# Optimization experiments

Measured on AMD Instinct MI355X. Metric: run time of the kernel, lower is better.

Reference implementation:

```python
import jax, jax.numpy as jnp
import numpy as np
import math

N_HEAD = 16
N_EMBD = 1024
HEAD_D = N_EMBD // N_HEAD
BASE = 10000


def rope(Y):
    # Y: [b, h, t, d]; positions start at 1 as in the torch code
    d = Y.shape[-1]
    t = Y.shape[-2]
    theta = BASE ** (-2.0 * jnp.arange(d // 2, dtype=Y.dtype) / d)
    theta2 = jnp.concatenate([theta, theta], axis=0)          # [d]
    pos = jnp.arange(1, t + 1, dtype=Y.dtype)                 # [t]
    C = pos[:, None] * theta2[None, :]                        # [t, d]
    cos, sin = jnp.cos(C), jnp.sin(C)
    Y2 = jnp.concatenate([-Y[..., d // 2:], Y[..., : d // 2]], axis=-1)
    return Y * cos + Y2 * sin


def setup_inputs() -> dict:
    key = jax.random.key(0)
    ks = jax.random.split(key, 9)
    s = 0.02
    x = jax.random.normal(ks[0], (4, 2048, N_EMBD), dtype=jnp.float32)
    Wq = jax.random.normal(ks[1], (N_EMBD, N_EMBD), dtype=jnp.float32) * s
    bq = jnp.zeros((N_EMBD,), dtype=jnp.float32)
    Wk = jax.random.normal(ks[2], (N_EMBD, N_EMBD), dtype=jnp.float32) * s
    bk = jnp.zeros((N_EMBD,), dtype=jnp.float32)
    Wv = jax.random.normal(ks[3], (N_EMBD, N_EMBD), dtype=jnp.float32) * s
    bv = jnp.zeros((N_EMBD,), dtype=jnp.float32)
    Wo = jax.random.normal(ks[4], (N_EMBD, N_EMBD), dtype=jnp.float32) * s
    bo = jnp.zeros((N_EMBD,), dtype=jnp.float32)
    return {"x": x, "Wq": Wq, "bq": bq, "Wk": Wk, "bk": bk,
            "Wv": Wv, "bv": bv, "Wo": Wo, "bo": bo}


def reference(x, Wq, bq, Wk, bk, Wv, bv, Wo, bo):
    b, t, _ = x.shape
    def split_heads(y):
        return y.reshape(b, t, N_HEAD, HEAD_D).transpose(0, 2, 1, 3)  # b h t d
    q = split_heads(x @ Wq.T + bq)
    k = split_heads(x @ Wk.T + bk)
    v = split_heads(x @ Wv.T + bv)
    q, k = rope(q), rope(k)
    scale = math.sqrt(HEAD_D)
    att = jnp.einsum('bhqd,bhkd->bhqk', q, k) / scale
    mask = jnp.tril(jnp.ones((t, t), dtype=bool))
    att = jnp.where(mask, att, -jnp.inf)
    att = jax.nn.softmax(att, axis=-1)
    y = jnp.einsum('bhqk,bhkd->bhqd', att, v)
    y = y.transpose(0, 2, 1, 3).reshape(b, t, N_EMBD)
    return y @ Wo.T + bo
```

## Files before the change

kernel.cpp:

```cpp
#include <hip/hip_runtime.h>
#include <hip/hip_bf16.h>
#include <cstdint>

typedef __attribute__((ext_vector_type(8))) short short8;
typedef __attribute__((ext_vector_type(4))) short short4v;
typedef __attribute__((ext_vector_type(4))) float f32x4;
typedef __attribute__((ext_vector_type(16))) float f32x16;
typedef __attribute__((ext_vector_type(4))) unsigned int u32x4;
typedef unsigned short ushort_t;
typedef unsigned int uint32;

#define DEVI static __device__ __forceinline__

DEVI ushort_t f2bf(float f){
  uint32 u = __builtin_bit_cast(uint32, f);
  u += 0x7FFFu + ((u >> 16) & 1u);
  return (ushort_t)(u >> 16);
}
DEVI float bf2f(ushort_t s){
  uint32 u = ((uint32)s) << 16;
  return __builtin_bit_cast(float, u);
}
DEVI uint32 cvtpk_bf16(float lo, float hi){
  uint32 r;
  asm("v_cvt_pk_bf16_f32 %0, %1, %2" : "=v"(r) : "v"(lo), "v"(hi));
  return r;
}
DEVI void plswap(uint32& a, uint32& b){
  asm("v_permlane32_swap_b32 %0, %1" : "+v"(a), "+v"(b));
}

typedef __attribute__((address_space(1))) const uint32 g_u32;
typedef __attribute__((address_space(3))) uint32 l_u32;
#define GL_LDS16(gp, lp) __builtin_amdgcn_global_load_lds((g_u32*)(gp), (l_u32*)(lp), 16, 0, 0)

__global__ __launch_bounds__(256) void convert_all(
    const float* __restrict__ x, const float* __restrict__ wq, const float* __restrict__ wk,
    const float* __restrict__ wv, const float* __restrict__ wo,
    ushort_t* __restrict__ xb, ushort_t* __restrict__ wqkv, ushort_t* __restrict__ wob){
  int bid = blockIdx.x;
  const float* src; ushort_t* dst; long base;
  if (bid < 4096){ src = x; dst = xb; base = (long)bid * 2048; }
  else {
    int r = bid - 4096; int sel = r >> 9; int o = r & 511;
    src = sel==0?wq: sel==1?wk: sel==2?wv: wo;
    dst = (sel<3) ? (wqkv + (long)sel * 1048576) : wob;
    base = (long)o * 2048;
  }
  long i = base + (long)threadIdx.x * 8;
  const float* p = src + i;
  float4 a = *(const float4*)p;
  float4 b = *(const float4*)(p + 4);
  short8 v;
  v[0]=(short)f2bf(a.x); v[1]=(short)f2bf(a.y); v[2]=(short)f2bf(a.z); v[3]=(short)f2bf(a.w);
  v[4]=(short)f2bf(b.x); v[5]=(short)f2bf(b.y); v[6]=(short)f2bf(b.z); v[7]=(short)f2bf(b.w);
  *(short8*)(dst + i) = v;
}

__global__ __launch_bounds__(256) void rope_table(float2* __restrict__ tab){
  const int idx = blockIdx.x * 256 + threadIdx.x;
  const int tok = idx >> 5, j = idx & 31;
  const float theta = exp2f(-(float)j * 0.4152410118609203f);
  const float ang = (float)(tok + 1) * theta;
  float s, c;
  sincosf(ang, &s, &c);
  tab[idx] = make_float2(c, s);
}

__global__ __launch_bounds__(256) void gemm_qkv(
    const ushort_t* __restrict__ A, const ushort_t* __restrict__ Bw,
    const float* __restrict__ bq, const float* __restrict__ bk, const float* __restrict__ bv,
    const float2* __restrict__ tab,
    ushort_t* __restrict__ Qb, ushort_t* __restrict__ Kb, ushort_t* __restrict__ Vt){
  __shared__ ushort_t As[4096];
  __shared__ ushort_t Bs[4096];
  const int tid = threadIdx.x, l = tid & 63, w = tid >> 6;
  const int lr = l & 15, lg = l >> 4;
  const int bid = (blockIdx.x & 7) * 192 + (blockIdx.x >> 3);
  const int bm = bid / 24, bn = bid % 24;
  const int m0 = bm << 7, n0 = bn << 7;
  const int wm = (w >> 1) << 6, wn = (w & 1) << 6;
  f32x4 acc[4][4] = {};
  const ushort_t* aS = A + (long)(m0 + (tid >> 2)) * 1024 + (tid & 3) * 8;
  const ushort_t* bS = Bw + (long)(n0 + (tid >> 2)) * 1024 + (tid & 3) * 8;
  const long skip = (long)64 * 1024;
  for (int kt = 0; kt < 32; ++kt){
    GL_LDS16(aS,        &As[w * 512]);
    GL_LDS16(aS + skip, &As[2048 + w * 512]);
    GL_LDS16(bS,        &Bs[w * 512]);
    GL_LDS16(bS + skip, &Bs[2048 + w * 512]);
    aS += 32; bS += 32;
    __syncthreads();
    short8 af[4], bfr[4];
#pragma unroll
    for (int mi = 0; mi < 4; ++mi) af[mi]  = *(const short8*)&As[(wm + mi*16 + lr)*32 + lg*8];
#pragma unroll
    for (int ni = 0; ni < 4; ++ni) bfr[ni] = *(const short8*)&Bs[(wn + ni*16 + lr)*32 + lg*8];
#pragma unroll
    for (int mi = 0; mi < 4; ++mi)
#pragma unroll
      for (int ni = 0; ni < 4; ++ni)
        acc[mi][ni] = __builtin_amdgcn_mfma_f32_16x16x32_bf16(af[mi], bfr[ni], acc[mi][ni], 0, 0, 0);
    __syncthreads();
  }
  const int sel = bn >> 3;
  const int h = ((n0 + wn) >> 6) & 15;
  const int colBase = n0 + wn + lr;
  if (sel < 2){
    ushort_t* dst = (sel == 0) ? Qb : Kb;
    const float* bp = (sel == 0) ? bq : bk;
    const float bvs[4] = {bp[colBase], bp[colBase+16], bp[colBase+32], bp[colBase+48]};
#pragma unroll
    for (int mi = 0; mi < 4; ++mi){
      const int row0 = m0 + wm + mi*16 + lg*4;
#pragma unroll
      for (int i = 0; i < 4; ++i){
        const int r = row0 + i;
        const int b = r >> 11, tok = r & 2047;
#pragma unroll
        for (int nip = 0; nip < 2; ++nip){
          const int j = lr + nip*16;
          const float2 cs = tab[tok*32 + j];
          const float v0 = acc[mi][nip][i]   + bvs[nip];
          const float v1 = acc[mi][nip+2][i] + bvs[nip+2];
          const long base = (((long)(b*16 + h) * 2048 + tok) << 6) + j;
          dst[base]      = f2bf(v0 * cs.x - v1 * cs.y);
          dst[base + 32] = f2bf(v1 * cs.x + v0 * cs.y);
        }
      }
    }
  } else {
    const float bvs[4] = {bv[colBase], bv[colBase+16], bv[colBase+32], bv[colBase+48]};
#pragma unroll
    for (int mi = 0; mi < 4; ++mi){
      const int row0 = m0 + wm + mi*16 + lg*4;
#pragma unroll
      for (int ni = 0; ni < 4; ++ni){
        const int d = lr + ni*16;
#pragma unroll
        for (int i = 0; i < 4; ++i){
          const int r = row0 + i;
          const int b = r >> 11, tok = r & 2047;
          Vt[((long)(b*16 + h) * 64 + d) * 2048 + tok] = f2bf(acc[mi][ni][i] + bvs[ni]);
        }
      }
    }
  }
}

__global__ __launch_bounds__(256) void gemm_out(
    const ushort_t* __restrict__ A, const ushort_t* __restrict__ Bw,
    const float* __restrict__ bias, float* __restrict__ Cout){
  __shared__ ushort_t As[4096];
  __shared__ ushort_t Bs[4096];
  const int tid = threadIdx.x, l = tid & 63, w = tid >> 6;
  const int lr = l & 15, lg = l >> 4;
  const int bid = (blockIdx.x & 7) * 64 + (blockIdx.x >> 3);
  const int bm = bid >> 3, bn = bid & 7;
  const int m0 = bm << 7, n0 = bn << 7;
  const int wm = (w >> 1) << 6, wn = (w & 1) << 6;
  f32x4 acc[4][4] = {};
  const ushort_t* aS = A + (long)(m0 + (tid >> 2)) * 1024 + (tid & 3) * 8;
  const ushort_t* bS = Bw + (long)(n0 + (tid >> 2)) * 1024 + (tid & 3) * 8;
  const long skip = (long)64 * 1024;
  for (int kt = 0; kt < 32; ++kt){
    GL_LDS16(aS,        &As[w * 512]);
    GL_LDS16(aS + skip, &As[2048 + w * 512]);
    GL_LDS16(bS,        &Bs[w * 512]);
    GL_LDS16(bS + skip, &Bs[2048 + w * 512]);
    aS += 32; bS += 32;
    __syncthreads();
    short8 af[4], bfr[4];
#pragma unroll
    for (int mi = 0; mi < 4; ++mi) af[mi]  = *(const short8*)&As[(wm + mi*16 + lr)*32 + lg*8];
#pragma unroll
    for (int ni = 0; ni < 4; ++ni) bfr[ni] = *(const short8*)&Bs[(wn + ni*16 + lr)*32 + lg*8];
#pragma unroll
    for (int mi = 0; mi < 4; ++mi)
#pragma unroll
      for (int ni = 0; ni < 4; ++ni)
        acc[mi][ni] = __builtin_amdgcn_mfma_f32_16x16x32_bf16(af[mi], bfr[ni], acc[mi][ni], 0, 0, 0);
    __syncthreads();
  }
  const int colBase = n0 + wn + lr;
#pragma unroll
  for (int mi = 0; mi < 4; ++mi){
    const int row0 = m0 + wm + mi*16 + lg*4;
#pragma unroll
    for (int ni = 0; ni < 4; ++ni){
      const int col = colBase + ni*16;
      const float bvv = bias[col];
#pragma unroll
      for (int i = 0; i < 4; ++i)
        Cout[(long)(row0 + i) * 1024 + col] = acc[mi][ni][i] + bvv;
    }
  }
}

__global__ __launch_bounds__(512, 4) void attn(
    const ushort_t* __restrict__ Qb, const ushort_t* __restrict__ Kb,
    const ushort_t* __restrict__ Vt, ushort_t* __restrict__ yb){
  __shared__ __align__(16) ushort_t Ks[2][2048];
  __shared__ __align__(16) ushort_t Vs[2][2048];
  const int tid = threadIdx.x;
  const int w = tid >> 6, l = tid & 63;
  const int lq = l & 31;
  const int hi = l >> 5;
  const int xcd = blockIdx.x & 7;
  const int idx = blockIdx.x >> 3;
  const int hi5 = idx >> 5;
  const int bh  = (xcd << 3) + ((idx >> 3) & 3) + hi5 * 4;
  const int qj  = hi5 ? (idx & 7) : 7 - (idx & 7);
  const int qc = (qj << 3) + w;
  const int q0 = qc << 5;
  const int ktmax = (qj << 3) + 7;
  const ushort_t* Qh = Qb + (long)bh * 2048 * 64;
  const ushort_t* Kh = Kb + (long)bh * 2048 * 64;
  const ushort_t* Vth = Vt + (long)bh * 64 * 2048;
  const int h8 = hi * 8;

  const ushort_t* qp = &Qh[(long)(q0 + lq) * 64 + h8];
  short8 qf0 = *(const short8*)(qp);
  short8 qf1 = *(const short8*)(qp + 16);
  short8 qf2 = *(const short8*)(qp + 32);
  short8 qf3 = *(const short8*)(qp + 48);

  const int stg_is_v = (w >= 4);
  long stg_src_off; int stg_dst_off;
  if (!stg_is_v){
    const int row = (w << 3) + (l >> 3);
    const int cl  = (l & 7) ^ (row & 7);
    stg_src_off = ((long)row << 6) + (cl << 3);
    stg_dst_off = (w << 9) + (l << 3);
  } else {
    const int row = ((w - 4) << 3) + (l >> 3);
    const int cl  = (l & 7) ^ (row & 7);
    const int dd  = row + ((cl & 4) << 3);
    stg_src_off = ((long)dd << 11) + ((cl & 3) << 3);
    stg_dst_off = ((w - 4) << 9) + (l << 3);
  }

  f32x16 o0 = {}, o1 = {};
  float lsum = 0.f;
  const float cl2 = 0.1803368801111204f;

  if (!stg_is_v) GL_LDS16(Kh + stg_src_off,  &Ks[0][stg_dst_off]);
  else           GL_LDS16(Vth + stg_src_off, &Vs[0][stg_dst_off]);
  __syncthreads();

  int cur = 0;
  for (int kt = 0; kt <= ktmax; ++kt){
    if (kt < ktmax){
      const int k0n = (kt + 1) << 5;
      if (!stg_is_v) GL_LDS16(Kh + ((long)k0n << 6) + stg_src_off, &Ks[cur ^ 1][stg_dst_off]);
      else           GL_LDS16(Vth + k0n + stg_src_off,             &Vs[cur ^ 1][stg_dst_off]);
    }
    if (kt <= qc){
      const int swk = lq & 7;
      const ushort_t* kr = &Ks[cur][lq << 6];
      short8 kf0 = *(const short8*)&kr[((hi    ) ^ swk) << 3];
      short8 kf1 = *(const short8*)&kr[((2 + hi) ^ swk) << 3];
      short8 kf2 = *(const short8*)&kr[((4 + hi) ^ swk) << 3];
      short8 kf3 = *(const short8*)&kr[((6 + hi) ^ swk) << 3];
      const ushort_t* vr = &Vs[cur][lq << 6];
      short8 vf00 = *(const short8*)&vr[((hi    ) ^ swk) << 3];
      short8 vf01 = *(const short8*)&vr[((2 + hi) ^ swk) << 3];
      short8 vf10 = *(const short8*)&vr[((4 + hi) ^ swk) << 3];
      short8 vf11 = *(const short8*)&vr[((6 + hi) ^ swk) << 3];
      f32x16 s = {};
      s = __builtin_amdgcn_mfma_f32_32x32x16_bf16(kf0, qf0, s, 0, 0, 0);
      s = __builtin_amdgcn_mfma_f32_32x32x16_bf16(kf1, qf1, s, 0, 0, 0);
      s = __builtin_amdgcn_mfma_f32_32x32x16_bf16(kf2, qf2, s, 0, 0, 0);
      s = __builtin_amdgcn_mfma_f32_32x32x16_bf16(kf3, qf3, s, 0, 0, 0);
      if (kt == qc){
#pragma unroll
        for (int r = 0; r < 16; ++r){
          const int rk = (r & 3) + 8 * (r >> 2) + 4 * hi;
          if (rk > lq) s[r] = -1e30f;
        }
      }
#pragma unroll
      for (int r = 0; r < 16; ++r) s[r] = __builtin_amdgcn_exp2f(__builtin_fmaf(s[r], cl2, -2.0f));
      {
        float t0 = (s[0] + s[1]) + (s[2] + s[3]);
        float t1 = (s[4] + s[5]) + (s[6] + s[7]);
        float t2 = (s[8] + s[9]) + (s[10] + s[11]);
        float t3 = (s[12] + s[13]) + (s[14] + s[15]);
        lsum += (t0 + t1) + (t2 + t3);
      }
      uint32 a0 = cvtpk_bf16(s[0], s[1]),  b0 = cvtpk_bf16(s[4], s[5]);
      uint32 a1 = cvtpk_bf16(s[2], s[3]),  b1 = cvtpk_bf16(s[6], s[7]);
      uint32 a2 = cvtpk_bf16(s[8], s[9]),  b2 = cvtpk_bf16(s[12], s[13]);
      uint32 a3 = cvtpk_bf16(s[10], s[11]),b3 = cvtpk_bf16(s[14], s[15]);
      plswap(a0, b0);
      plswap(a1, b1);
      plswap(a2, b2);
      plswap(a3, b3);
      u32x4 pc0 = {a0, a1, b0, b1};
      u32x4 pc1 = {a2, a3, b2, b3};
      short8 pb0 = __builtin_bit_cast(short8, pc0);
      short8 pb1 = __builtin_bit_cast(short8, pc1);
      o0 = __builtin_amdgcn_mfma_f32_32x32x16_bf16(vf00, pb0, o0, 0, 0, 0);
      o0 = __builtin_amdgcn_mfma_f32_32x32x16_bf16(vf01, pb1, o0, 0, 0, 0);
      o1 = __builtin_amdgcn_mfma_f32_32x32x16_bf16(vf10, pb0, o1, 0, 0, 0);
      o1 = __builtin_amdgcn_mfma_f32_32x32x16_bf16(vf11, pb1, o1, 0, 0, 0);
    }
    __syncthreads();
    cur ^= 1;
  }
  lsum += __shfl_xor(lsum, 32);
  const float inv = 1.0f / lsum;
  const int b = bh >> 4, h = bh & 15;
  const int tok = q0 + lq;
  ushort_t* yrow = yb + (long)(b * 2048 + tok) * 1024 + h * 64;
#pragma unroll
  for (int g = 0; g < 4; ++g){
    short4v p0, p1;
#pragma unroll
    for (int j = 0; j < 4; ++j){
      p0[j] = (short)f2bf(o0[4*g + j] * inv);
      p1[j] = (short)f2bf(o1[4*g + j] * inv);
    }
    *(short4v*)&yrow[8*g + 4*hi]      = p0;
    *(short4v*)&yrow[32 + 8*g + 4*hi] = p1;
  }
}

extern "C" void kernel_launch(void* const* d_in, const int* in_sizes, int n_in,
                              void* d_out, int out_size, void* d_ws, size_t ws_size,
                              hipStream_t stream){
  const float* x  = (const float*)d_in[0];
  const float* Wq = (const float*)d_in[1];
  const float* bq = (const float*)d_in[2];
  const float* Wk = (const float*)d_in[3];
  const float* bk = (const float*)d_in[4];
  const float* Wv = (const float*)d_in[5];
  const float* bv = (const float*)d_in[6];
  const float* Wo = (const float*)d_in[7];
  const float* bo = (const float*)d_in[8];
  char* ws = (char*)d_ws;
  ushort_t* xb   = (ushort_t*)(ws);
  ushort_t* wqkv = (ushort_t*)(ws + 16777216);
  ushort_t* wob  = (ushort_t*)(ws + 23068672);
  float2*   tab  = (float2*)  (ws + 25165824);
  ushort_t* Qb   = (ushort_t*)(ws + 25690112);
  ushort_t* Kb   = (ushort_t*)(ws + 42467328);
  ushort_t* Vt   = (ushort_t*)(ws + 59244544);
  ushort_t* yb   = xb;

  convert_all<<<6144, 256, 0, stream>>>(x, Wq, Wk, Wv, Wo, xb, wqkv, wob);
  rope_table<<<256, 256, 0, stream>>>(tab);
  gemm_qkv<<<1536, 256, 0, stream>>>(xb, wqkv, bq, bk, bv, tab, Qb, Kb, Vt);
  attn<<<512, 512, 0, stream>>>(Qb, Kb, Vt, yb);
  gemm_out<<<512, 256, 0, stream>>>(yb, wob, bo, (float*)d_out);
}
```

Measured before the change: 170.8 us.

## Rewrite QKV GEMM with 256x256 tiles, triple-buffered LDS and swizzle

Replaces the 128x128 QKV projection GEMM with a 256x256-tile kernel of 512 threads (8 waves) that triple-buffers its LDS stages. It issues global-to-LDS loads two k-steps ahead, splits each k-step into two MFMA phases with barriers and s_setprio, and XOR-swizzles the LDS layout to avoid bank conflicts. The aim is better reuse of each loaded tile and overlap of memory latency with compute. It uses about 96KB of LDS and more accumulator registers per thread, which limits occupancy, and gives fewer blocks (384) across the CUs.

```diff
diff --git a/kernel.cpp b/kernel.cpp
--- a/kernel.cpp
+++ b/kernel.cpp
@@ -67,81 +67,114 @@
   tab[idx] = make_float2(c, s);
 }
 
-__global__ __launch_bounds__(256) void gemm_qkv(
+__global__ __launch_bounds__(512, 2) void gemm256_qkv(
     const ushort_t* __restrict__ A, const ushort_t* __restrict__ Bw,
     const float* __restrict__ bq, const float* __restrict__ bk, const float* __restrict__ bv,
     const float2* __restrict__ tab,
     ushort_t* __restrict__ Qb, ushort_t* __restrict__ Kb, ushort_t* __restrict__ Vt){
-  __shared__ ushort_t As[4096];
-  __shared__ ushort_t Bs[4096];
-  const int tid = threadIdx.x, l = tid & 63, w = tid >> 6;
-  const int lr = l & 15, lg = l >> 4;
-  const int bid = (blockIdx.x & 7) * 192 + (blockIdx.x >> 3);
-  const int bm = bid / 24, bn = bid % 24;
-  const int m0 = bm << 7, n0 = bn << 7;
-  const int wm = (w >> 1) << 6, wn = (w & 1) << 6;
-  f32x4 acc[4][4] = {};
-  const ushort_t* aS = A + (long)(m0 + (tid >> 2)) * 1024 + (tid & 3) * 8;
-  const ushort_t* bS = Bw + (long)(n0 + (tid >> 2)) * 1024 + (tid & 3) * 8;
-  const long skip = (long)64 * 1024;
-  for (int kt = 0; kt < 32; ++kt){
-    GL_LDS16(aS,        &As[w * 512]);
-    GL_LDS16(aS + skip, &As[2048 + w * 512]);
-    GL_LDS16(bS,        &Bs[w * 512]);
-    GL_LDS16(bS + skip, &Bs[2048 + w * 512]);
-    aS += 32; bS += 32;
-    __syncthreads();
-    short8 af[4], bfr[4];
-#pragma unroll
-    for (int mi = 0; mi < 4; ++mi) af[mi]  = *(const short8*)&As[(wm + mi*16 + lr)*32 + lg*8];
-#pragma unroll
-    for (int ni = 0; ni < 4; ++ni) bfr[ni] = *(const short8*)&Bs[(wn + ni*16 + lr)*32 + lg*8];
-#pragma unroll
-    for (int mi = 0; mi < 4; ++mi)
-#pragma unroll
-      for (int ni = 0; ni < 4; ++ni)
-        acc[mi][ni] = __builtin_amdgcn_mfma_f32_16x16x32_bf16(af[mi], bfr[ni], acc[mi][ni], 0, 0, 0);
-    __syncthreads();
-  }
-  const int sel = bn >> 3;
-  const int h = ((n0 + wn) >> 6) & 15;
-  const int colBase = n0 + wn + lr;
+  __shared__ __align__(16) ushort_t S[49152];
+  const int tid = threadIdx.x;
+  const int w = tid >> 6, l = tid & 63, lr = l & 15, lg = l >> 4;
+  const int wm = w >> 2, wn = w & 3;
+  const int bid = (blockIdx.x & 7) * 48 + (blockIdx.x >> 3);
+  const int bm = bid / 12, bn = bid % 12;
+  const int m0 = bm << 8, n0 = bn << 8;
+  const int srow = tid >> 2;
+  const int swzc = (tid & 3) ^ (srow & 3) ^ ((srow >> 2) & 3);
+  const ushort_t* aS = A  + (long)(m0 + srow) * 1024 + swzc * 8;
+  const ushort_t* bS = Bw + (long)(n0 + srow) * 1024 + swzc * 8;
+  const int sw = (lr & 3) ^ ((lr >> 2) & 3);
+  const int aOff = ((wm << 7) + lr) * 32 + ((lg ^ sw) << 3);
+  const int bOff = 8192 + ((wn << 6) + lr) * 32 + ((lg ^ sw) << 3);
+  f32x4 acc[8][4] = {};
+
+#define STG(matOff, src, t, bf_) do{ \
+    GL_LDS16((src) + (long)(t)*32,          &S[(bf_)*16384 + (matOff) + tid*8]); \
+    GL_LDS16((src) + (long)(t)*32 + 131072, &S[(bf_)*16384 + (matOff) + 4096 + tid*8]); }while(0)
+
+  STG(0, aS, 0, 0); STG(8192, bS, 0, 0);
+  STG(0, aS, 1, 1); STG(8192, bS, 1, 1);
+  asm volatile("s_waitcnt vmcnt(4)" ::: "memory");
+  __builtin_amdgcn_s_barrier();
+
+  int buf = 0;
+  for (int t = 0; t < 32; ++t){
+    const int nbuf = (buf == 0) ? 2 : buf - 1;
+    const ushort_t* Sb = &S[buf * 16384];
+    short8 af[8], bf0[2];
+#pragma unroll
+    for (int mi = 0; mi < 8; ++mi) af[mi] = *(const short8*)&Sb[aOff + mi * 512];
+    bf0[0] = *(const short8*)&Sb[bOff];
+    bf0[1] = *(const short8*)&Sb[bOff + 512];
+    if (t < 30) STG(0, aS, t + 2, nbuf);
+    __builtin_amdgcn_s_barrier();
+    __builtin_amdgcn_s_setprio(1);
+#pragma unroll
+    for (int mi = 0; mi < 8; ++mi){
+      acc[mi][0] = __builtin_amdgcn_mfma_f32_16x16x32_bf16(af[mi], bf0[0], acc[mi][0], 0, 0, 0);
+      acc[mi][1] = __builtin_amdgcn_mfma_f32_16x16x32_bf16(af[mi], bf0[1], acc[mi][1], 0, 0, 0);
+    }
+    __builtin_amdgcn_s_setprio(0);
+    __builtin_amdgcn_s_barrier();
+    short8 bf1[2];
+    bf1[0] = *(const short8*)&Sb[bOff + 1024];
+    bf1[1] = *(const short8*)&Sb[bOff + 1536];
+    if (t < 30) STG(8192, bS, t + 2, nbuf);
+    __builtin_amdgcn_s_barrier();
+    __builtin_amdgcn_s_setprio(1);
+#pragma unroll
+    for (int mi = 0; mi < 8; ++mi){
+      acc[mi][2] = __builtin_amdgcn_mfma_f32_16x16x32_bf16(af[mi], bf1[0], acc[mi][2], 0, 0, 0);
+      acc[mi][3] = __builtin_amdgcn_mfma_f32_16x16x32_bf16(af[mi], bf1[1], acc[mi][3], 0, 0, 0);
+    }
+    __builtin_amdgcn_s_setprio(0);
+    if (t < 30) asm volatile("s_waitcnt vmcnt(4)" ::: "memory");
+    else        asm volatile("s_waitcnt vmcnt(0)" ::: "memory");
+    __builtin_amdgcn_s_barrier();
+    buf = (buf == 2) ? 0 : buf + 1;
+  }
+#undef STG
+
+  const int colX = n0 + (wn << 6);
+  const int sel = colX >> 10;
+  const int h = (colX >> 6) & 15;
+  const int cB = (colX & 1023) + lr;
   if (sel < 2){
-    ushort_t* dst = (sel == 0) ? Qb : Kb;
-    const float* bp = (sel == 0) ? bq : bk;
-    const float bvs[4] = {bp[colBase], bp[colBase+16], bp[colBase+32], bp[colBase+48]};
-#pragma unroll
-    for (int mi = 0; mi < 4; ++mi){
-      const int row0 = m0 + wm + mi*16 + lg*4;
+    ushort_t* dst = sel ? Kb : Qb;
+    const float* bp = sel ? bk : bq;
+    const float bvs[4] = {bp[cB], bp[cB+16], bp[cB+32], bp[cB+48]};
+#pragma unroll
+    for (int mi = 0; mi < 8; ++mi){
+      const int row0 = m0 + (wm << 7) + mi*16 + lg*4;
 #pragma unroll
       for (int i = 0; i < 4; ++i){
         const int r = row0 + i;
         const int b = r >> 11, tok = r & 2047;
 #pragma unroll
-        for (int nip = 0; nip < 2; ++nip){
-          const int j = lr + nip*16;
+        for (int nc = 0; nc < 2; ++nc){
+          const int j = nc*16 + lr;
           const float2 cs = tab[tok*32 + j];
-          const float v0 = acc[mi][nip][i]   + bvs[nip];
-          const float v1 = acc[mi][nip+2][i] + bvs[nip+2];
-          const long base = (((long)(b*16 + h) * 2048 + tok) << 6) + j;
+          const float v0 = acc[mi][nc][i]   + bvs[nc];
+          const float v1 = acc[mi][nc+2][i] + bvs[nc+2];
+          const long base = (((long)((b<<4) + h) * 2048 + tok) << 6) + j;
           dst[base]      = f2bf(v0 * cs.x - v1 * cs.y);
           dst[base + 32] = f2bf(v1 * cs.x + v0 * cs.y);
         }
       }
     }
   } else {
-    const float bvs[4] = {bv[colBase], bv[colBase+16], bv[colBase+32], bv[colBase+48]};
-#pragma unroll
-    for (int mi = 0; mi < 4; ++mi){
-      const int row0 = m0 + wm + mi*16 + lg*4;
-#pragma unroll
-      for (int ni = 0; ni < 4; ++ni){
-        const int d = lr + ni*16;
+    const float bvs[4] = {bv[cB], bv[cB+16], bv[cB+32], bv[cB+48]};
+#pragma unroll
+    for (int mi = 0; mi < 8; ++mi){
+      const int row0 = m0 + (wm << 7) + mi*16 + lg*4;
+#pragma unroll
+      for (int nc = 0; nc < 4; ++nc){
+        const int d = nc*16 + lr;
 #pragma unroll
         for (int i = 0; i < 4; ++i){
           const int r = row0 + i;
           const int b = r >> 11, tok = r & 2047;
-          Vt[((long)(b*16 + h) * 64 + d) * 2048 + tok] = f2bf(acc[mi][ni][i] + bvs[ni]);
+          Vt[((long)((b<<4) + h) * 64 + d) * 2048 + tok] = f2bf(acc[mi][nc][i] + bvs[nc]);
         }
       }
     }
@@ -350,7 +383,7 @@
 
   convert_all<<<6144, 256, 0, stream>>>(x, Wq, Wk, Wv, Wo, xb, wqkv, wob);
   rope_table<<<256, 256, 0, stream>>>(tab);
-  gemm_qkv<<<1536, 256, 0, stream>>>(xb, wqkv, bq, bk, bv, tab, Qb, Kb, Vt);
+  gemm256_qkv<<<384, 512, 0, stream>>>(xb, wqkv, bq, bk, bv, tab, Qb, Kb, Vt);
   attn<<<512, 512, 0, stream>>>(Qb, Kb, Vt, yb);
   gemm_out<<<512, 256, 0, stream>>>(yb, wob, bo, (float*)d_out);
 }
```

After: 171.3 us. No clear change (+0.2%).
